# Kernel optimization log

Measured on AMD Instinct MI355X. Metric: run time of the kernel, lower is better.

Reference implementation:

```python
import jax, jax.numpy as jnp
import numpy as np

N_NODES = 50000
HIDDEN = 256
N_EDGES = 800000


def setup_inputs() -> dict:
    key = jax.random.key(0)
    k_z, k_e, k_w1, k_b1, k_w2, k_b2 = jax.random.split(key, 6)
    z = jax.random.normal(k_z, (N_NODES, HIDDEN), dtype=jnp.float32)
    edge_index = jax.random.randint(k_e, (2, N_EDGES), 0, N_NODES, dtype=jnp.int64)
    # Linear params stored as (in, out); scaled like torch default init
    W1 = jax.random.normal(k_w1, (2 * HIDDEN, HIDDEN), dtype=jnp.float32) * (1.0 / np.sqrt(2 * HIDDEN))
    b1 = jax.random.normal(k_b1, (HIDDEN,), dtype=jnp.float32) * 0.01
    W2 = jax.random.normal(k_w2, (HIDDEN, 1), dtype=jnp.float32) * (1.0 / np.sqrt(HIDDEN))
    b2 = jax.random.normal(k_b2, (1,), dtype=jnp.float32) * 0.01
    return {"z": z, "edge_index": edge_index, "W1": W1, "b1": b1, "W2": W2, "b2": b2}


def reference(z, edge_index, W1, b1, W2, b2):
    src = edge_index[0]
    dst = edge_index[1]
    # gather endpoints and concat: [E, 2*H]
    edge_feat = jnp.concatenate([z[src], z[dst]], axis=1)
    x = jnp.dot(edge_feat, W1) + b1          # [E, H]
    x = jax.nn.relu(x)
    score = jnp.dot(x, W2) + b2              # [E, 1]
    return score
```

## Files before the change

kernel.cpp:

```cpp
#include <hip/hip_runtime.h>
#include <hip/hip_bf16.h>

#define NN 50000
#define HID 256
#define NE 800000

typedef unsigned short u16;
typedef __attribute__((ext_vector_type(8))) short short8v;
typedef __attribute__((ext_vector_type(4))) float f32x4;

__device__ __forceinline__ u16 f2bf(float v) {
    __hip_bfloat16 h = __float2bfloat16(v);
    return *reinterpret_cast<u16*>(&h);
}

__global__ __launch_bounds__(256)
void prep_w1b(const float* __restrict__ W1, u16* __restrict__ W1b) {
    const int idx = blockIdx.x * 256 + threadIdx.x;
    if (idx >= 32 * 512) return;
    const int kbg  = idx >> 9;
    const int j    = idx & 511;
    const int row0 = (j >= HID) ? HID : 0;
    const int col  = j & (HID - 1);
    u16 o[8];
    #pragma unroll
    for (int kk = 0; kk < 8; ++kk) {
        const int k = kbg * 8 + kk;
        o[kk] = f2bf(W1[(size_t)(row0 + k) * HID + col]);
    }
    *(uint4*)(W1b + (size_t)idx * 8) = *(uint4*)o;
}

#define BM 128
#define BN 128
#define BK 32
#define LDE 136

__global__ __launch_bounds__(256)
void node_gemm(const float* __restrict__ z, const u16* __restrict__ W1b,
               const float* __restrict__ b1, u16* __restrict__ P) {
    __shared__ __align__(16) u16 lds[BM * LDE];

    const int tid  = threadIdx.x;
    const int lane = tid & 63;
    const int wid  = tid >> 6;
    const int wr   = wid >> 1;
    const int wc   = wid & 1;
    const int m0 = blockIdx.y * BM;
    const int j0 = blockIdx.x * BN;

    const int l16 = lane & 15;
    const int l4  = lane >> 4;

    const int ar  = tid >> 3;
    const int ac4 = (tid & 7) * 4;
    const int akb = ac4 >> 3;
    const int akk = ac4 & 7;

    f32x4 acc[4][4] = {};

    for (int k0 = 0; k0 < HID; k0 += BK) {
        float4 av[4];
        #pragma unroll
        for (int q = 0; q < 4; ++q) {
            const int r  = q * 32 + ar;
            const int gm = m0 + r;
            av[q] = (gm < NN) ? *(const float4*)(z + (size_t)gm * HID + k0 + ac4)
                              : make_float4(0.f, 0.f, 0.f, 0.f);
        }
        uint4 bv[2];
        #pragma unroll
        for (int h = 0; h < 2; ++h) {
            const int kb = h * 2 + (tid >> 7);
            const int j  = tid & 127;
            bv[h] = *(const uint4*)(W1b + ((size_t)((k0 >> 3) + kb) * 512 + j0 + j) * 8);
        }
        __syncthreads();
        #pragma unroll
        for (int q = 0; q < 4; ++q) {
            const int r = q * 32 + ar;
            u16 pk[4] = { f2bf(av[q].x), f2bf(av[q].y), f2bf(av[q].z), f2bf(av[q].w) };
            *(uint2*)&lds[akb * (BM * 8) + r * 8 + akk] = *(uint2*)pk;
        }
        #pragma unroll
        for (int h = 0; h < 2; ++h) {
            const int kb = h * 2 + (tid >> 7);
            const int j  = tid & 127;
            *(uint4*)&lds[4096 + kb * (BN * 8) + j * 8] = bv[h];
        }
        __syncthreads();
        short8v a[4], b[4];
        #pragma unroll
        for (int mi = 0; mi < 4; ++mi)
            a[mi] = *(short8v*)&lds[l4 * (BM * 8) + (wr * 64 + mi * 16 + l16) * 8];
        #pragma unroll
        for (int ni = 0; ni < 4; ++ni)
            b[ni] = *(short8v*)&lds[4096 + l4 * (BN * 8) + (wc * 64 + ni * 16 + l16) * 8];
        #pragma unroll
        for (int mi = 0; mi < 4; ++mi)
            #pragma unroll
            for (int ni = 0; ni < 4; ++ni)
                acc[mi][ni] = __builtin_amdgcn_mfma_f32_16x16x32_bf16(
                    a[mi], b[ni], acc[mi][ni], 0, 0, 0);
    }

    float bvals[4];
    #pragma unroll
    for (int ni = 0; ni < 4; ++ni) {
        const int col = j0 + wc * 64 + ni * 16 + l16;
        bvals[ni] = (col < HID) ? b1[col] : 0.f;
    }
    __syncthreads();
    #pragma unroll
    for (int mi = 0; mi < 4; ++mi) {
        const int rbase = wr * 64 + mi * 16 + l4 * 4;
        #pragma unroll
        for (int ni = 0; ni < 4; ++ni) {
            const int c = wc * 64 + ni * 16 + l16;
            #pragma unroll
            for (int r = 0; r < 4; ++r)
                lds[(rbase + r) * LDE + c] = f2bf(acc[mi][ni][r] + bvals[ni]);
        }
    }
    __syncthreads();
    #pragma unroll
    for (int it = 0; it < 8; ++it) {
        const int flat = it * 256 + tid;
        const int row  = flat >> 4;
        const int g    = flat & 15;
        const int gm   = m0 + row;
        if (gm < NN)
            *(uint4*)(P + (size_t)gm * 512 + j0 + g * 8) = *(uint4*)&lds[row * LDE + g * 8];
    }
}

__device__ __forceinline__ void proc_pair(unsigned int ua, unsigned int ub,
                                          float w0, float w1, float& s) {
    const float a0 = __uint_as_float(ua << 16);
    const float a1 = __uint_as_float(ua & 0xffff0000u);
    const float b0 = __uint_as_float(ub << 16);
    const float b1 = __uint_as_float(ub & 0xffff0000u);
    const float x0 = fmaxf(a0 + b0, 0.f);
    const float x1 = fmaxf(a1 + b1, 0.f);
    s = fmaf(x0, w0, s);
    s = fmaf(x1, w1, s);
}

__global__ __launch_bounds__(256)
void edge_kernel(const int* __restrict__ ei, const u16* __restrict__ P,
                 const float* __restrict__ W2, const float* __restrict__ b2,
                 float* __restrict__ out) {
    const int lane = threadIdx.x & 63;
    const int sub  = lane >> 4;
    const int l16  = lane & 15;
    const int h0   = l16 * 16;

    float w[16];
    #pragma unroll
    for (int i = 0; i < 16; i += 4) {
        const float4 v = *(const float4*)(W2 + h0 + i);
        w[i] = v.x; w[i + 1] = v.y; w[i + 2] = v.z; w[i + 3] = v.w;
    }
    const float bias2 = b2[0];

    const int gwave   = (blockIdx.x * blockDim.x + threadIdx.x) >> 6;
    const int nwaves  = (gridDim.x * blockDim.x) >> 6;
    const int ngroups = NE >> 2;

    for (int g = gwave; g < ngroups; g += nwaves) {
        const int e   = g * 4 + sub;
        const int src = ei[e];
        const int dst = ei[NE + e];

        const u16* pa = P + (size_t)src * 512 + h0;
        const u16* pb = P + (size_t)dst * 512 + 256 + h0;
        const uint4 ta0 = *(const uint4*)(pa);
        const uint4 ta1 = *(const uint4*)(pa + 8);
        const uint4 tb0 = *(const uint4*)(pb);
        const uint4 tb1 = *(const uint4*)(pb + 8);

        float s = 0.f;
        proc_pair(ta0.x, tb0.x, w[0],  w[1],  s);
        proc_pair(ta0.y, tb0.y, w[2],  w[3],  s);
        proc_pair(ta0.z, tb0.z, w[4],  w[5],  s);
        proc_pair(ta0.w, tb0.w, w[6],  w[7],  s);
        proc_pair(ta1.x, tb1.x, w[8],  w[9],  s);
        proc_pair(ta1.y, tb1.y, w[10], w[11], s);
        proc_pair(ta1.z, tb1.z, w[12], w[13], s);
        proc_pair(ta1.w, tb1.w, w[14], w[15], s);

        s += __shfl_xor(s, 1);
        s += __shfl_xor(s, 2);
        s += __shfl_xor(s, 4);
        s += __shfl_xor(s, 8);
        if (l16 == 0) out[e] = s + bias2;
    }
}

extern "C" void kernel_launch(void* const* d_in, const int* in_sizes, int n_in,
                              void* d_out, int out_size, void* d_ws, size_t ws_size,
                              hipStream_t stream) {
    const float* z  = (const float*)d_in[0];
    const int*   ei = (const int*)d_in[1];
    const float* W1 = (const float*)d_in[2];
    const float* b1 = (const float*)d_in[3];
    const float* W2 = (const float*)d_in[4];
    const float* b2 = (const float*)d_in[5];
    float* out = (float*)d_out;

    u16* W1b = (u16*)d_ws;
    u16* P   = (u16*)d_ws + 131072;

    prep_w1b<<<64, 256, 0, stream>>>(W1, W1b);

    dim3 g1(4, (NN + BM - 1) / BM);
    node_gemm<<<g1, 256, 0, stream>>>(z, W1b, b1, P);

    edge_kernel<<<2048, 256, 0, stream>>>(ei, P, W2, b2, out);
}
```

Baseline: 284.6 us.

## Restructure node GEMM to register-resident A rows with B streamed from global

The node GEMM now gives each block 64 rows and all 512 output columns. Each wave keeps its 16 z rows, converted to bf16, in registers across the whole K range and reads W1 fragments directly from global or L2 instead of staging A and B tiles through LDS with barriers. This removes the LDS staging and syncthreads in the K loop, and z is read once rather than four times, once per column tile. In exchange every wave re-reads all of W1b from cache, and the wave-private LDS store and readback in the epilogue has no barrier between them.

```diff
diff --git a/kernel.cpp b/kernel.cpp
--- a/kernel.cpp
+++ b/kernel.cpp
@@ -31,106 +31,65 @@
     *(uint4*)(W1b + (size_t)idx * 8) = *(uint4*)o;
 }
 
-#define BM 128
-#define BN 128
-#define BK 32
 #define LDE 136
 
 __global__ __launch_bounds__(256)
 void node_gemm(const float* __restrict__ z, const u16* __restrict__ W1b,
                const float* __restrict__ b1, u16* __restrict__ P) {
-    __shared__ __align__(16) u16 lds[BM * LDE];
+    __shared__ __align__(16) u16 lds[64 * LDE];
 
     const int tid  = threadIdx.x;
     const int lane = tid & 63;
-    const int wid  = tid >> 6;
-    const int wr   = wid >> 1;
-    const int wc   = wid & 1;
-    const int m0 = blockIdx.y * BM;
-    const int j0 = blockIdx.x * BN;
+    const int w    = tid >> 6;
+    const int l16  = lane & 15;
+    const int l4   = lane >> 4;
+    const int m0   = blockIdx.x * 64;
+    const int row  = m0 + w * 16 + l16;
 
-    const int l16 = lane & 15;
-    const int l4  = lane >> 4;
-
-    const int ar  = tid >> 3;
-    const int ac4 = (tid & 7) * 4;
-    const int akb = ac4 >> 3;
-    const int akk = ac4 & 7;
-
-    f32x4 acc[4][4] = {};
-
-    for (int k0 = 0; k0 < HID; k0 += BK) {
-        float4 av[4];
-        #pragma unroll
-        for (int q = 0; q < 4; ++q) {
-            const int r  = q * 32 + ar;
-            const int gm = m0 + r;
-            av[q] = (gm < NN) ? *(const float4*)(z + (size_t)gm * HID + k0 + ac4)
-                              : make_float4(0.f, 0.f, 0.f, 0.f);
+    short8v af[8];
+    const bool rowok = (row < NN);
+    const float* zr = z + (size_t)row * HID;
+    #pragma unroll
+    for (int ks = 0; ks < 8; ++ks) {
+        float4 v0 = make_float4(0.f, 0.f, 0.f, 0.f), v1 = v0;
+        if (rowok) {
+            v0 = *(const float4*)(zr + ks * 32 + l4 * 8);
+            v1 = *(const float4*)(zr + ks * 32 + l4 * 8 + 4);
         }
-        uint4 bv[2];
-        #pragma unroll
-        for (int h = 0; h < 2; ++h) {
-            const int kb = h * 2 + (tid >> 7);
-            const int j  = tid & 127;
-            bv[h] = *(const uint4*)(W1b + ((size_t)((k0 >> 3) + kb) * 512 + j0 + j) * 8);
-        }
-        __syncthreads();
-        #pragma unroll
-        for (int q = 0; q < 4; ++q) {
-            const int r = q * 32 + ar;
-            u16 pk[4] = { f2bf(av[q].x), f2bf(av[q].y), f2bf(av[q].z), f2bf(av[q].w) };
-            *(uint2*)&lds[akb * (BM * 8) + r * 8 + akk] = *(uint2*)pk;
-        }
-        #pragma unroll
-        for (int h = 0; h < 2; ++h) {
-            const int kb = h * 2 + (tid >> 7);
-            const int j  = tid & 127;
-            *(uint4*)&lds[4096 + kb * (BN * 8) + j * 8] = bv[h];
-        }
-        __syncthreads();
-        short8v a[4], b[4];
-        #pragma unroll
-        for (int mi = 0; mi < 4; ++mi)
-            a[mi] = *(short8v*)&lds[l4 * (BM * 8) + (wr * 64 + mi * 16 + l16) * 8];
-        #pragma unroll
-        for (int ni = 0; ni < 4; ++ni)
-            b[ni] = *(short8v*)&lds[4096 + l4 * (BN * 8) + (wc * 64 + ni * 16 + l16) * 8];
-        #pragma unroll
-        for (int mi = 0; mi < 4; ++mi)
-            #pragma unroll
-            for (int ni = 0; ni < 4; ++ni)
-                acc[mi][ni] = __builtin_amdgcn_mfma_f32_16x16x32_bf16(
-                    a[mi], b[ni], acc[mi][ni], 0, 0, 0);
+        u16 t[8] = { f2bf(v0.x), f2bf(v0.y), f2bf(v0.z), f2bf(v0.w),
+                     f2bf(v1.x), f2bf(v1.y), f2bf(v1.z), f2bf(v1.w) };
+        af[ks] = *(short8v*)t;
     }
 
-    float bvals[4];
-    #pragma unroll
-    for (int ni = 0; ni < 4; ++ni) {
-        const int col = j0 + wc * 64 + ni * 16 + l16;
-        bvals[ni] = (col < HID) ? b1[col] : 0.f;
-    }
-    __syncthreads();
-    #pragma unroll
-    for (int mi = 0; mi < 4; ++mi) {
-        const int rbase = wr * 64 + mi * 16 + l4 * 4;
+    for (int jt = 0; jt < 4; ++jt) {
+        f32x4 acc[8] = {};
+        const u16* bbase = W1b + ((size_t)l4 * 512 + jt * 128 + l16) * 8;
         #pragma unroll
-        for (int ni = 0; ni < 4; ++ni) {
-            const int c = wc * 64 + ni * 16 + l16;
+        for (int ks = 0; ks < 8; ++ks) {
+            #pragma unroll
+            for (int ni = 0; ni < 8; ++ni) {
+                const short8v b = *(const short8v*)(bbase + ((size_t)ks * 4 * 512 + ni * 16) * 8);
+                acc[ni] = __builtin_amdgcn_mfma_f32_16x16x32_bf16(af[ks], b, acc[ni], 0, 0, 0);
+            }
+        }
+
+        #pragma unroll
+        for (int ni = 0; ni < 8; ++ni) {
+            const float bias = (jt < 2) ? b1[jt * 128 + ni * 16 + l16] : 0.f;
             #pragma unroll
             for (int r = 0; r < 4; ++r)
-                lds[(rbase + r) * LDE + c] = f2bf(acc[mi][ni][r] + bvals[ni]);
+                lds[(w * 16 + l4 * 4 + r) * LDE + ni * 16 + l16] =
+                    f2bf(acc[ni][r] + bias);
         }
-    }
-    __syncthreads();
-    #pragma unroll
-    for (int it = 0; it < 8; ++it) {
-        const int flat = it * 256 + tid;
-        const int row  = flat >> 4;
-        const int g    = flat & 15;
-        const int gm   = m0 + row;
-        if (gm < NN)
-            *(uint4*)(P + (size_t)gm * 512 + j0 + g * 8) = *(uint4*)&lds[row * LDE + g * 8];
+        const int crow = w * 16 + (lane >> 2);
+        const int ccol = (lane & 3) * 32;
+        const int gm   = m0 + crow;
+        if (gm < NN) {
+            u16* dst = P + (size_t)gm * 512 + jt * 128 + ccol;
+            #pragma unroll
+            for (int q = 0; q < 4; ++q)
+                *(uint4*)(dst + q * 8) = *(uint4*)&lds[crow * LDE + ccol + q * 8];
+        }
     }
 }
 
@@ -213,8 +172,7 @@
 
     prep_w1b<<<64, 256, 0, stream>>>(W1, W1b);
 
-    dim3 g1(4, (NN + BM - 1) / BM);
-    node_gemm<<<g1, 256, 0, stream>>>(z, W1b, b1, P);
+    node_gemm<<<(NN + 63) / 64, 256, 0, stream>>>(z, W1b, b1, P);
 
     edge_kernel<<<2048, 256, 0, stream>>>(ei, P, W2, b2, out);
 }
```

Result: no change. 289.9 us (+1.9%).
